# Optimization experiments

Hardware: AMD Instinct MI355X
Metric: run time of the kernel (lower is better)

The kernel has to match this reference:

```python
import jax, jax.numpy as jnp
import numpy as np

MAX_LENGTH = 13
PAD_TOKEN = 0
HIDDEN = 1024
VOCAB = 32000
BATCH = 64


def gru_cell(x, h, w_ih, w_hh, b_ih, b_hh):
    # PyTorch GRU gate order: reset, update, new
    gi = x @ w_ih.T + b_ih            # [B, 3H]
    gh = h @ w_hh.T + b_hh            # [B, 3H]
    i_r, i_z, i_n = jnp.split(gi, 3, axis=-1)
    h_r, h_z, h_n = jnp.split(gh, 3, axis=-1)
    r = jax.nn.sigmoid(i_r + h_r)
    z = jax.nn.sigmoid(i_z + h_z)
    n = jnp.tanh(i_n + r * h_n)
    return (1.0 - z) * n + z * h


def setup_inputs() -> dict:
    key = jax.random.key(0)
    ks = jax.random.split(key, 9)
    s = 0.02
    return {
        "encoder_outputs": jax.random.normal(ks[0], (BATCH, MAX_LENGTH, HIDDEN), jnp.float32),
        "encoder_hidden": jax.random.normal(ks[1], (1, BATCH, HIDDEN), jnp.float32),
        "embedding": jax.random.normal(ks[2], (VOCAB, HIDDEN), jnp.float32) * s,
        "w_ih": jax.random.normal(ks[3], (3 * HIDDEN, HIDDEN), jnp.float32) * s,
        "w_hh": jax.random.normal(ks[4], (3 * HIDDEN, HIDDEN), jnp.float32) * s,
        "b_ih": jnp.zeros((3 * HIDDEN,), jnp.float32),
        "b_hh": jnp.zeros((3 * HIDDEN,), jnp.float32),
        "w_out": jax.random.normal(ks[5], (VOCAB, HIDDEN), jnp.float32) * s,
        "b_out": jnp.zeros((VOCAB,), jnp.float32),
    }


def reference(encoder_outputs, encoder_hidden, embedding, w_ih, w_hh, b_ih, b_hh, w_out, b_out):
    batch = encoder_outputs.shape[0]
    h0 = encoder_hidden[0]                               # [B, H]
    tok0 = jnp.full((batch,), PAD_TOKEN, dtype=jnp.int32)

    def step(carry, _):
        h, tok = carry
        x = jax.nn.relu(embedding[tok])                  # embed + relu
        h = gru_cell(x, h, w_ih, w_hh, b_ih, b_hh)       # GRU cell
        logits = h @ w_out.T + b_out                     # [B, V]
        nxt = jnp.argmax(logits, axis=-1).astype(jnp.int32)  # greedy feedback (topk(1))
        return (h, nxt), logits

    (h_final, _), logits = jax.lax.scan(step, (h0, tok0), None, length=MAX_LENGTH)
    logits = jnp.transpose(logits, (1, 0, 2))            # [B, T, V]
    log_probs = jax.nn.log_softmax(logits, axis=-1)
    return log_probs, h_final[None]
```

## Files before the change

### kernel.cpp

```cpp
#include <hip/hip_runtime.h>
#include <math.h>

#define BB 64
#define HH 1024
#define VV 32000
#define TT 13
#define QS 8000
#define BKL 128

typedef float f32x4 __attribute__((ext_vector_type(4)));
typedef __bf16 bf16x8 __attribute__((ext_vector_type(8)));

__device__ __forceinline__ unsigned short f2bf(float f) {
  unsigned u = __float_as_uint(f);
  u = (u + 0x7fffu + ((u >> 16) & 1u)) >> 16;
  return (unsigned short)u;
}
__device__ __forceinline__ float bf2f(unsigned short s) {
  return __uint_as_float(((unsigned)s) << 16);
}

__device__ __forceinline__ void gld16(const void* g, void* l) {
  __builtin_amdgcn_global_load_lds(
      (const __attribute__((address_space(1))) unsigned int*)g,
      (__attribute__((address_space(3))) unsigned int*)l, 16, 0, 0);
}

__global__ __launch_bounds__(1024) void k_init(
    const float* __restrict__ enc, const float* __restrict__ emb,
    float* __restrict__ hrm, unsigned short* __restrict__ hhi,
    unsigned short* __restrict__ hlo, unsigned short* __restrict__ xhi,
    unsigned short* __restrict__ xlo) {
  const int g = blockIdx.x * 1024 + threadIdx.x;
  const float h = enc[g];
  hrm[g] = h;
  const unsigned short h16 = f2bf(h);
  hhi[g] = h16;
  hlo[g] = f2bf(h - bf2f(h16));
  float e = emb[threadIdx.x];
  e = e > 0.f ? e : 0.f;
  const unsigned short e16 = f2bf(e);
  xhi[g] = e16;
  xlo[g] = f2bf(e - bf2f(e16));
}

__global__ __launch_bounds__(256) void k_wconv(const float* __restrict__ w,
                                               unsigned short* __restrict__ o) {
  const int n4 = VV * HH / 4;
  for (int i = blockIdx.x * 256 + threadIdx.x; i < n4; i += gridDim.x * 256) {
    const f32x4 v = ((const f32x4*)w)[i];
    ushort4 u;
    u.x = f2bf(v[0]); u.y = f2bf(v[1]); u.z = f2bf(v[2]); u.w = f2bf(v[3]);
    ((ushort4*)o)[i] = u;
  }
}

__global__ __launch_bounds__(256) void k_wconv2(
    const float* __restrict__ wih, const float* __restrict__ whh,
    unsigned short* __restrict__ ghi, unsigned short* __restrict__ glo) {
  const int n4 = 6 * HH * HH / 4;
  for (int i = blockIdx.x * 256 + threadIdx.x; i < n4; i += gridDim.x * 256) {
    const int flat = i * 4;
    const float* src = flat < 3 * HH * HH ? wih + flat : whh + (flat - 3 * HH * HH);
    const f32x4 v = *(const f32x4*)src;
    ushort4 hi, lo;
    hi.x = f2bf(v[0]); lo.x = f2bf(v[0] - bf2f(hi.x));
    hi.y = f2bf(v[1]); lo.y = f2bf(v[1] - bf2f(hi.y));
    hi.z = f2bf(v[2]); lo.z = f2bf(v[2] - bf2f(hi.z));
    hi.w = f2bf(v[3]); lo.w = f2bf(v[3] - bf2f(hi.w));
    ((ushort4*)ghi)[i] = hi;
    ((ushort4*)glo)[i] = lo;
  }
}

__global__ __launch_bounds__(256) void k_wconv3(
    const float* __restrict__ emb, unsigned short* __restrict__ ehi,
    unsigned short* __restrict__ elo) {
  const int n4 = VV * HH / 4;
  for (int i = blockIdx.x * 256 + threadIdx.x; i < n4; i += gridDim.x * 256) {
    f32x4 v = ((const f32x4*)emb)[i];
    #pragma unroll
    for (int u = 0; u < 4; ++u) v[u] = v[u] > 0.f ? v[u] : 0.f;
    ushort4 hi, lo;
    hi.x = f2bf(v[0]); lo.x = f2bf(v[0] - bf2f(hi.x));
    hi.y = f2bf(v[1]); lo.y = f2bf(v[1] - bf2f(hi.y));
    hi.z = f2bf(v[2]); lo.z = f2bf(v[2] - bf2f(hi.z));
    hi.w = f2bf(v[3]); lo.w = f2bf(v[3] - bf2f(hi.w));
    ((ushort4*)ehi)[i] = hi;
    ((ushort4*)elo)[i] = lo;
  }
}

__global__ __launch_bounds__(64) void k_gruG(
    const unsigned short* __restrict__ ehi, const unsigned short* __restrict__ elo,
    const unsigned short* __restrict__ hhi_s, const unsigned short* __restrict__ hlo_s,
    const unsigned short* __restrict__ ghi, const unsigned short* __restrict__ glo,
    const float* __restrict__ qbestV, const int* __restrict__ qbestI,
    float* __restrict__ gbuf, int use_qbest) {
  __shared__ int stok[64];
  const int blk = blockIdx.x, lane = threadIdx.x;
  const int kh = blk & 1;
  const int r2 = blk >> 1;
  const int g6 = r2 % 6, jt = r2 / 6;
  const int cl = lane & 15, kk = (lane >> 4) * 8;
  const int j = jt * 16 + cl;
  const int kbeg = kh * 512;
  const bool ih = g6 < 3;

  if (ih) {
    int tok = 0;
    if (use_qbest) {
      float bv = qbestV[lane * 4 + 0]; int bi = qbestI[lane * 4 + 0];
      #pragma unroll
      for (int qq = 1; qq < 4; ++qq) {
        const float v = qbestV[lane * 4 + qq]; const int i2 = qbestI[lane * 4 + qq];
        if (v > bv || (v == bv && i2 < bi)) { bv = v; bi = i2; }
      }
      tok = bi;
    }
    stok[lane] = tok;
  }
  __syncthreads();

  size_t abase[4];
  #pragma unroll
  for (int rt = 0; rt < 4; ++rt) {
    const int row = rt * 16 + cl;
    abase[rt] = (ih ? (size_t)stok[row] : (size_t)row) * HH + kbeg + kk;
  }
  const unsigned short* Ahi = ih ? ehi : hhi_s;
  const unsigned short* Alo = ih ? elo : hlo_s;
  const unsigned short* bh = ghi + (size_t)(g6 * HH + j) * HH + kbeg;
  const unsigned short* bl = glo + (size_t)(g6 * HH + j) * HH + kbeg;

  f32x4 acc[4];
  acc[0] = acc[1] = acc[2] = acc[3] = (f32x4){0.f, 0.f, 0.f, 0.f};
  #pragma unroll 4
  for (int k0 = 0; k0 < 512; k0 += 32) {
    const bf16x8 whi = *(const bf16x8*)(bh + k0 + kk);
    const bf16x8 wlo = *(const bf16x8*)(bl + k0 + kk);
    #pragma unroll
    for (int rt = 0; rt < 4; ++rt) {
      const bf16x8 a_h = *(const bf16x8*)(Ahi + abase[rt] + k0);
      const bf16x8 a_l = *(const bf16x8*)(Alo + abase[rt] + k0);
      acc[rt] = __builtin_amdgcn_mfma_f32_16x16x32_bf16(a_h, whi, acc[rt], 0, 0, 0);
      acc[rt] = __builtin_amdgcn_mfma_f32_16x16x32_bf16(a_l, whi, acc[rt], 0, 0, 0);
      acc[rt] = __builtin_amdgcn_mfma_f32_16x16x32_bf16(a_h, wlo, acc[rt], 0, 0, 0);
    }
  }
  #pragma unroll
  for (int rt = 0; rt < 4; ++rt)
    #pragma unroll
    for (int rg = 0; rg < 4; ++rg) {
      const int row = rt * 16 + (lane >> 4) * 4 + rg;
      gbuf[(size_t)((kh * 6 + g6) * BB + row) * HH + jt * 16 + cl] = acc[rt][rg];
    }
}

__global__ __launch_bounds__(256) void k_gepO(
    const float* __restrict__ gbuf, const float* __restrict__ bih,
    const float* __restrict__ bhh, const float* __restrict__ hsrc,
    float* __restrict__ hdst, unsigned short* __restrict__ hhi_d,
    unsigned short* __restrict__ hlo_d,
    const float* __restrict__ lbufPrev, const float* __restrict__ mq,
    const float* __restrict__ sq, float* __restrict__ out, int t) {
  __shared__ float lz[BB];
  const int tid = threadIdx.x;
  const int gid = blockIdx.x * 256 + tid;
  if (t > 0 && tid < BB) {
    const int b = tid;
    const float m0 = mq[b * 4 + 0], m1 = mq[b * 4 + 1];
    const float m2 = mq[b * 4 + 2], m3 = mq[b * 4 + 3];
    const float Mg = fmaxf(fmaxf(m0, m1), fmaxf(m2, m3));
    const float Sg = sq[b * 4 + 0] * __expf(m0 - Mg) + sq[b * 4 + 1] * __expf(m1 - Mg) +
                     sq[b * 4 + 2] * __expf(m2 - Mg) + sq[b * 4 + 3] * __expf(m3 - Mg);
    lz[b] = Mg + logf(Sg);
  }
  __syncthreads();
  {
    const int b = gid >> 10, j = gid & (HH - 1);
    const size_t base = (size_t)b * HH + j;
    const float gir = gbuf[(size_t)(0 * BB + b) * HH + j] + gbuf[(size_t)((6 + 0) * BB + b) * HH + j] + bih[j];
    const float giz = gbuf[(size_t)(1 * BB + b) * HH + j] + gbuf[(size_t)((6 + 1) * BB + b) * HH + j] + bih[HH + j];
    const float gin = gbuf[(size_t)(2 * BB + b) * HH + j] + gbuf[(size_t)((6 + 2) * BB + b) * HH + j] + bih[2 * HH + j];
    const float ghr = gbuf[(size_t)(3 * BB + b) * HH + j] + gbuf[(size_t)((6 + 3) * BB + b) * HH + j] + bhh[j];
    const float ghz = gbuf[(size_t)(4 * BB + b) * HH + j] + gbuf[(size_t)((6 + 4) * BB + b) * HH + j] + bhh[HH + j];
    const float ghn = gbuf[(size_t)(5 * BB + b) * HH + j] + gbuf[(size_t)((6 + 5) * BB + b) * HH + j] + bhh[2 * HH + j];
    const float r_ = 1.f / (1.f + __expf(-(gir + ghr)));
    const float z_ = 1.f / (1.f + __expf(-(giz + ghz)));
    const float n_ = tanhf(gin + r_ * ghn);
    const float hnew = (1.f - z_) * n_ + z_ * hsrc[base];
    hdst[base] = hnew;
    const unsigned short h16 = f2bf(hnew);
    hhi_d[base] = h16;
    hlo_d[base] = f2bf(hnew - bf2f(h16));
  }
  if (t > 0) {
    const f32x4* src = (const f32x4*)lbufPrev;
    for (int i4 = gid; i4 < BB * VV / 4; i4 += 65536) {
      const int b = i4 / (VV / 4);
      const f32x4 v = src[i4];
      ((f32x4*)out)[(size_t)(b * TT + (t - 1)) * (VV / 4) + (i4 - b * (VV / 4))] = v - lz[b];
    }
  }
}

__global__ __launch_bounds__(512, 1) void k_logits_lds(
    const unsigned short* __restrict__ hb,
    const unsigned short* __restrict__ wbf,
    const float* __restrict__ bout, float* __restrict__ lbuf) {
  __shared__ __attribute__((aligned(16))) unsigned char sA[2][64 * BKL * 2];
  __shared__ __attribute__((aligned(16))) unsigned char sB[2][128 * BKL * 2];
  const int tid = threadIdx.x, blk = blockIdx.x;
  const int lane = tid & 63, wv = tid >> 6;
  const int cl = lane & 15, kk = (lane >> 4) * 8;

  auto STAGE = [&](int buf, int k0) {
    #pragma unroll
    for (int it = 0; it < 2; ++it) {
      const int c = it * 512 + tid;
      const int r = c >> 4;
      const int kb = (c & 15) * 16;
      const int kbs = kb ^ ((r & 7) << 4);
      gld16(hb + (size_t)r * HH + k0 + (kbs >> 1),
            &sA[buf][it * 8192 + wv * 1024]);
    }
    #pragma unroll
    for (int it = 0; it < 4; ++it) {
      const int c = it * 512 + tid;
      const int col = c >> 4;
      const int kb = (c & 15) * 16;
      const int kbs = kb ^ ((col & 7) << 4);
      gld16(wbf + (size_t)(blk * 128 + col) * HH + k0 + (kbs >> 1),
            &sB[buf][it * 8192 + wv * 1024]);
    }
  };

  f32x4 acc[4];
  acc[0] = acc[1] = acc[2] = acc[3] = (f32x4){0.f, 0.f, 0.f, 0.f};

  STAGE(0, 0);
  for (int t = 0; t < HH / BKL; ++t) {
    const int cur = t & 1;
    if (t < HH / BKL - 1) {
      STAGE(cur ^ 1, (t + 1) * BKL);
      asm volatile("s_waitcnt vmcnt(6)" ::: "memory");
    } else {
      asm volatile("s_waitcnt vmcnt(0)" ::: "memory");
    }
    __builtin_amdgcn_s_barrier();
    __builtin_amdgcn_sched_barrier(0);
    #pragma unroll
    for (int ks = 0; ks < BKL; ks += 32) {
      const int bc = wv * 16 + cl;
      const bf16x8 bfr = *(const bf16x8*)&sB[cur][bc * (BKL * 2) + (((ks + kk) * 2) ^ ((bc & 7) << 4))];
      #pragma unroll
      for (int rt = 0; rt < 4; ++rt) {
        const int ar = rt * 16 + cl;
        const bf16x8 afr = *(const bf16x8*)&sA[cur][ar * (BKL * 2) + (((ks + kk) * 2) ^ ((ar & 7) << 4))];
        acc[rt] = __builtin_amdgcn_mfma_f32_16x16x32_bf16(afr, bfr, acc[rt], 0, 0, 0);
      }
    }
    __builtin_amdgcn_s_barrier();
    __builtin_amdgcn_sched_barrier(0);
  }

  const int col = blk * 128 + wv * 16 + cl;
  const float bo = bout[col];
  #pragma unroll
  for (int rt = 0; rt < 4; ++rt)
    #pragma unroll
    for (int rg = 0; rg < 4; ++rg) {
      const int row = rt * 16 + (lane >> 4) * 4 + rg;
      lbuf[(size_t)row * VV + col] = acc[rt][rg] + bo;
    }
}

__global__ __launch_bounds__(256) void k_sum(
    const float* __restrict__ lbuf, const float* __restrict__ wout,
    const float* __restrict__ bout, const float* __restrict__ hnew,
    float* __restrict__ mq, float* __restrict__ sq,
    float* __restrict__ qbestV, int* __restrict__ qbestI, int dorecheck) {
  __shared__ float srow[QS];
  __shared__ float red[4];
  __shared__ int icnt;
  __shared__ int scand[32];
  const int tid = threadIdx.x;
  const int b = blockIdx.x >> 2, q = blockIdx.x & 3;
  const int lane = tid & 63, wv = tid >> 6;
  const f32x4* src = (const f32x4*)(lbuf + (size_t)b * VV + q * QS);
  f32x4* s4 = (f32x4*)srow;

  float m = -3.0e38f;
  for (int i = tid; i < QS / 4; i += 256) {
    const f32x4 v = src[i];
    s4[i] = v;
    m = fmaxf(fmaxf(fmaxf(m, v[0]), v[1]), fmaxf(v[2], v[3]));
  }
  #pragma unroll
  for (int d = 1; d < 64; d <<= 1) m = fmaxf(m, __shfl_xor(m, d, 64));
  if (lane == 0) red[wv] = m;
  if (tid == 0) icnt = 0;
  __syncthreads();
  const float M = fmaxf(fmaxf(red[0], red[1]), fmaxf(red[2], red[3]));

  float s = 0.f;
  for (int i = tid; i < QS / 4; i += 256) {
    const f32x4 v = s4[i];
    s += __expf(v[0] - M) + __expf(v[1] - M) + __expf(v[2] - M) + __expf(v[3] - M);
  }
  #pragma unroll
  for (int d = 1; d < 64; d <<= 1) s += __shfl_xor(s, d, 64);
  __syncthreads();
  if (lane == 0) red[wv] = s;
  __syncthreads();
  if (tid == 0) {
    mq[b * 4 + q] = M;
    sq[b * 4 + q] = red[0] + red[1] + red[2] + red[3];
  }

  if (dorecheck) {
    const float thr = M - 0.05f;
    for (int i = tid; i < QS / 4; i += 256) {
      const f32x4 v = s4[i];
      #pragma unroll
      for (int u = 0; u < 4; ++u)
        if (v[u] >= thr) {
          const int c = atomicAdd(&icnt, 1);
          if (c < 32) scand[c] = q * QS + 4 * i + u;
        }
    }
    __syncthreads();
    if (wv == 0) {
      const int nc = icnt < 32 ? icnt : 32;
      const float* hrow = hnew + (size_t)b * HH;
      f32x4 h4[4];
      #pragma unroll
      for (int u = 0; u < 4; ++u) h4[u] = *(const f32x4*)(hrow + lane * 16 + u * 4);
      float best = -3.0e38f; int bi = 0x7fffffff;
      for (int ci = 0; ci < nc; ++ci) {
        const int v = scand[ci];
        const float* wrow = wout + (size_t)v * HH + lane * 16;
        float ss = 0.f;
        #pragma unroll
        for (int u = 0; u < 4; ++u) {
          const f32x4 w4 = *(const f32x4*)(wrow + u * 4);
          ss += h4[u][0] * w4[0] + h4[u][1] * w4[1] + h4[u][2] * w4[2] + h4[u][3] * w4[3];
        }
        #pragma unroll
        for (int d = 1; d < 64; d <<= 1) ss += __shfl_xor(ss, d, 64);
        ss += bout[v];
        if (ss > best || (ss == best && v < bi)) { best = ss; bi = v; }
      }
      if (lane == 0) { qbestV[b * 4 + q] = best; qbestI[b * 4 + q] = bi; }
    }
  }
}

__global__ __launch_bounds__(256) void k_fin(
    const float* __restrict__ lbufLast, const float* __restrict__ mq,
    const float* __restrict__ sq, const float* __restrict__ hfin,
    float* __restrict__ out) {
  __shared__ float lz[BB];
  const int tid = threadIdx.x;
  const int gid = blockIdx.x * 256 + tid;
  if (tid < BB) {
    const int b = tid;
    const float m0 = mq[b * 4 + 0], m1 = mq[b * 4 + 1];
    const float m2 = mq[b * 4 + 2], m3 = mq[b * 4 + 3];
    const float Mg = fmaxf(fmaxf(m0, m1), fmaxf(m2, m3));
    const float Sg = sq[b * 4 + 0] * __expf(m0 - Mg) + sq[b * 4 + 1] * __expf(m1 - Mg) +
                     sq[b * 4 + 2] * __expf(m2 - Mg) + sq[b * 4 + 3] * __expf(m3 - Mg);
    lz[b] = Mg + logf(Sg);
  }
  __syncthreads();
  const f32x4* src = (const f32x4*)lbufLast;
  for (int i4 = gid; i4 < BB * VV / 4; i4 += 65536) {
    const int b = i4 / (VV / 4);
    const f32x4 v = src[i4];
    ((f32x4*)out)[(size_t)(b * TT + (TT - 1)) * (VV / 4) + (i4 - b * (VV / 4))] = v - lz[b];
  }
  out[(size_t)BB * TT * VV + gid] = hfin[gid];
}

__global__ __launch_bounds__(64) void k_gru_fb(
    const unsigned short* __restrict__ xhi, const unsigned short* __restrict__ xlo,
    const unsigned short* __restrict__ hhi_s, const unsigned short* __restrict__ hlo_s,
    const float* __restrict__ wih, const float* __restrict__ whh,
    float* __restrict__ gbuf) {
  const int blk = blockIdx.x, lane = threadIdx.x;
  const int kh = blk & 1;
  const int r2 = blk >> 1;
  const int g6 = r2 % 6, jt = r2 / 6;
  const unsigned short* Ahi = g6 < 3 ? xhi : hhi_s;
  const unsigned short* Alo = g6 < 3 ? xlo : hlo_s;
  const int cl = lane & 15, kk = (lane >> 4) * 8;
  const int j = jt * 16 + cl;
  const int kbeg = kh * 512;
  f32x4 acc[4];
  acc[0] = acc[1] = acc[2] = acc[3] = (f32x4){0.f, 0.f, 0.f, 0.f};
  const float* W = (g6 < 3 ? wih : whh) + (size_t)((g6 % 3) * HH + j) * HH + kbeg;
  for (int k0 = 0; k0 < 512; k0 += 32) {
    const f32x4 w0 = *(const f32x4*)(W + k0 + kk);
    const f32x4 w1 = *(const f32x4*)(W + k0 + kk + 4);
    union { unsigned short u[8]; bf16x8 b; } chi, clo;
    #pragma unroll
    for (int u2 = 0; u2 < 4; ++u2) {
      chi.u[u2] = f2bf(w0[u2]); clo.u[u2] = f2bf(w0[u2] - bf2f(chi.u[u2]));
      chi.u[4 + u2] = f2bf(w1[u2]); clo.u[4 + u2] = f2bf(w1[u2] - bf2f(chi.u[4 + u2]));
    }
    #pragma unroll
    for (int rt = 0; rt < 4; ++rt) {
      const size_t aoff = (size_t)(rt * 16 + cl) * HH + kbeg + k0 + kk;
      const bf16x8 a_h = *(const bf16x8*)(Ahi + aoff);
      const bf16x8 a_l = *(const bf16x8*)(Alo + aoff);
      acc[rt] = __builtin_amdgcn_mfma_f32_16x16x32_bf16(a_h, chi.b, acc[rt], 0, 0, 0);
      acc[rt] = __builtin_amdgcn_mfma_f32_16x16x32_bf16(a_l, chi.b, acc[rt], 0, 0, 0);
      acc[rt] = __builtin_amdgcn_mfma_f32_16x16x32_bf16(a_h, clo.b, acc[rt], 0, 0, 0);
    }
  }
  #pragma unroll
  for (int rt = 0; rt < 4; ++rt)
    #pragma unroll
    for (int rg = 0; rg < 4; ++rg) {
      const int row = rt * 16 + (lane >> 4) * 4 + rg;
      gbuf[(size_t)((kh * 6 + g6) * BB + row) * HH + jt * 16 + cl] = acc[rt][rg];
    }
}

__global__ __launch_bounds__(256) void k_gep_fb(
    const float* __restrict__ gbuf, const float* __restrict__ bih,
    const float* __restrict__ bhh, const float* __restrict__ hsrc,
    float* __restrict__ hdst, unsigned short* __restrict__ hhi_d,
    unsigned short* __restrict__ hlo_d) {
  const int e = blockIdx.x * 256 + threadIdx.x;
  const int b = e >> 10, j = e & (HH - 1);
  const size_t base = (size_t)b * HH + j;
  const float gir = gbuf[(size_t)(0 * BB + b) * HH + j] + gbuf[(size_t)((6 + 0) * BB + b) * HH + j] + bih[j];
  const float giz = gbuf[(size_t)(1 * BB + b) * HH + j] + gbuf[(size_t)((6 + 1) * BB + b) * HH + j] + bih[HH + j];
  const float gin = gbuf[(size_t)(2 * BB + b) * HH + j] + gbuf[(size_t)((6 + 2) * BB + b) * HH + j] + bih[2 * HH + j];
  const float ghr = gbuf[(size_t)(3 * BB + b) * HH + j] + gbuf[(size_t)((6 + 3) * BB + b) * HH + j] + bhh[j];
  const float ghz = gbuf[(size_t)(4 * BB + b) * HH + j] + gbuf[(size_t)((6 + 4) * BB + b) * HH + j] + bhh[HH + j];
  const float ghn = gbuf[(size_t)(5 * BB + b) * HH + j] + gbuf[(size_t)((6 + 5) * BB + b) * HH + j] + bhh[2 * HH + j];
  const float r_ = 1.f / (1.f + __expf(-(gir + ghr)));
  const float z_ = 1.f / (1.f + __expf(-(giz + ghz)));
  const float n_ = tanhf(gin + r_ * ghn);
  const float hnew = (1.f - z_) * n_ + z_ * hsrc[base];
  hdst[base] = hnew;
  const unsigned short h16 = f2bf(hnew);
  hhi_d[base] = h16;
  hlo_d[base] = f2bf(hnew - bf2f(h16));
}

__global__ __launch_bounds__(256) void k_logits_fb(
    const unsigned short* __restrict__ hb, const float* __restrict__ wout,
    const float* __restrict__ bout, float* __restrict__ lbuf) {
  const int tid = threadIdx.x, blk = blockIdx.x;
  const int lane = tid & 63, wv = tid >> 6;
  const int n0 = blk * 64 + wv * 16;
  const int cl = lane & 15, kk = (lane >> 4) * 8;
  f32x4 acc[4];
  acc[0] = acc[1] = acc[2] = acc[3] = (f32x4){0.f, 0.f, 0.f, 0.f};
  const float* wrow = wout + (size_t)(n0 + cl) * HH;
  for (int k0 = 0; k0 < HH; k0 += 32) {
    const f32x4 w0 = *(const f32x4*)(wrow + k0 + kk);
    const f32x4 w1 = *(const f32x4*)(wrow + k0 + kk + 4);
    union { unsigned short u[8]; bf16x8 b; } cv;
    #pragma unroll
    for (int u2 = 0; u2 < 4; ++u2) { cv.u[u2] = f2bf(w0[u2]); cv.u[4 + u2] = f2bf(w1[u2]); }
    #pragma unroll
    for (int rt = 0; rt < 4; ++rt) {
      const bf16x8 afr = *(const bf16x8*)(hb + (size_t)(rt * 16 + cl) * HH + k0 + kk);
      acc[rt] = __builtin_amdgcn_mfma_f32_16x16x32_bf16(afr, cv.b, acc[rt], 0, 0, 0);
    }
  }
  const int col = n0 + cl;
  const float bo = bout[col];
  #pragma unroll
  for (int rt = 0; rt < 4; ++rt)
    #pragma unroll
    for (int rg = 0; rg < 4; ++rg) {
      const int row = rt * 16 + (lane >> 4) * 4 + rg;
      lbuf[(size_t)row * VV + col] = acc[rt][rg] + bo;
    }
}

__global__ __launch_bounds__(256) void k_out_fb(
    const float* __restrict__ lbuf, const float* __restrict__ mq,
    const float* __restrict__ sq, const float* __restrict__ qbestV,
    const int* __restrict__ qbestI, const float* __restrict__ emb,
    const float* __restrict__ hnew, float* __restrict__ out,
    unsigned short* __restrict__ xhi, unsigned short* __restrict__ xlo, int t) {
  __shared__ int stok;
  const int tid = threadIdx.x;
  const int b = blockIdx.x >> 2, q = blockIdx.x & 3;
  const float m0 = mq[b * 4 + 0], m1 = mq[b * 4 + 1];
  const float m2 = mq[b * 4 + 2], m3 = mq[b * 4 + 3];
  const float Mg = fmaxf(fmaxf(m0, m1), fmaxf(m2, m3));
  const float Sg = sq[b * 4 + 0] * __expf(m0 - Mg) + sq[b * 4 + 1] * __expf(m1 - Mg) +
                   sq[b * 4 + 2] * __expf(m2 - Mg) + sq[b * 4 + 3] * __expf(m3 - Mg);
  const float LZ = Mg + logf(Sg);
  const f32x4* src = (const f32x4*)(lbuf + (size_t)b * VV + q * QS);
  f32x4* dst = (f32x4*)(out + ((size_t)b * TT + t) * VV + q * QS);
  for (int i = tid; i < QS / 4; i += 256)
    dst[i] = src[i] - LZ;
  if (q == 0 && t < TT - 1) {
    if (tid == 0) {
      float bv = qbestV[b * 4 + 0]; int bi = qbestI[b * 4 + 0];
      #pragma unroll
      for (int qq = 1; qq < 4; ++qq) {
        const float v = qbestV[b * 4 + qq]; const int i2 = qbestI[b * 4 + qq];
        if (v > bv || (v == bv && i2 < bi)) { bv = v; bi = i2; }
      }
      stok = bi;
    }
    __syncthreads();
    const int tok = stok;
    for (int j = tid; j < HH; j += 256) {
      float e = emb[(size_t)tok * HH + j];
      e = e > 0.f ? e : 0.f;
      const unsigned short e16 = f2bf(e);
      xhi[(size_t)b * HH + j] = e16;
      xlo[(size_t)b * HH + j] = f2bf(e - bf2f(e16));
    }
  }
  if (q == 0 && t == TT - 1) {
    for (int j = tid; j < HH; j += 256)
      out[(size_t)BB * TT * VV + (size_t)b * HH + j] = hnew[(size_t)b * HH + j];
  }
}

extern "C" void kernel_launch(void* const* d_in, const int* in_sizes, int n_in,
                              void* d_out, int out_size, void* d_ws, size_t ws_size,
                              hipStream_t stream) {
  const float* enc  = (const float*)d_in[1];
  const float* emb  = (const float*)d_in[2];
  const float* wih  = (const float*)d_in[3];
  const float* whh  = (const float*)d_in[4];
  const float* bih  = (const float*)d_in[5];
  const float* bhh  = (const float*)d_in[6];
  const float* wout = (const float*)d_in[7];
  const float* bout = (const float*)d_in[8];
  float* out = (float*)d_out;

  char* ws = (char*)d_ws;
  size_t off = 0;
  auto alloc = [&](size_t bytes) -> char* {
    char* p = ws + off;
    off += (bytes + 255) & ~(size_t)255;
    return p;
  };
  float* hrm = (float*)alloc((size_t)2 * BB * HH * 4);
  unsigned short* hhi = (unsigned short*)alloc((size_t)2 * BB * HH * 2);
  unsigned short* hlo = (unsigned short*)alloc((size_t)2 * BB * HH * 2);
  unsigned short* xhi = (unsigned short*)alloc((size_t)BB * HH * 2);
  unsigned short* xlo = (unsigned short*)alloc((size_t)BB * HH * 2);
  float* gbuf = (float*)alloc((size_t)12 * BB * HH * 4);
  float* lbuf = (float*)alloc((size_t)2 * BB * VV * 4);
  float* mq = (float*)alloc((size_t)BB * 4 * 4);
  float* sq = (float*)alloc((size_t)BB * 4 * 4);
  float* qbestV = (float*)alloc((size_t)BB * 4 * 4);
  int* qbestI = (int*)alloc((size_t)BB * 4 * 4);
  unsigned short* wbf = (unsigned short*)alloc((size_t)VV * HH * 2);
  unsigned short* ghi = (unsigned short*)alloc((size_t)6 * HH * HH * 2);
  unsigned short* glo = (unsigned short*)alloc((size_t)6 * HH * HH * 2);
  unsigned short* ehi = (unsigned short*)alloc((size_t)VV * HH * 2);
  unsigned short* elo = (unsigned short*)alloc((size_t)VV * HH * 2);
  const int cache_ok = (ws_size >= off) ? 1 : 0;

  hipLaunchKernelGGL(k_init, dim3(64), dim3(1024), 0, stream,
                     enc, emb, hrm, hhi, hlo, xhi, xlo);
  if (cache_ok) {
    hipLaunchKernelGGL(k_wconv, dim3(2048), dim3(256), 0, stream, wout, wbf);
    hipLaunchKernelGGL(k_wconv2, dim3(1024), dim3(256), 0, stream, wih, whh, ghi, glo);
    hipLaunchKernelGGL(k_wconv3, dim3(2048), dim3(256), 0, stream, emb, ehi, elo);
  }

  for (int t = 0; t < TT; ++t) {
    const int p = t & 1;
    const float* hsrc = hrm + (size_t)p * BB * HH;
    float* hdst = hrm + (size_t)(p ^ 1) * BB * HH;
    const unsigned short* hhs = hhi + (size_t)p * BB * HH;
    const unsigned short* hls = hlo + (size_t)p * BB * HH;
    unsigned short* hhd = hhi + (size_t)(p ^ 1) * BB * HH;
    unsigned short* hld = hlo + (size_t)(p ^ 1) * BB * HH;
    float* lb = lbuf + (size_t)(t & 1) * BB * VV;
    const float* lbPrev = lbuf + (size_t)((t & 1) ^ 1) * BB * VV;

    if (cache_ok) {
      hipLaunchKernelGGL(k_gruG, dim3(768), dim3(64), 0, stream,
                         ehi, elo, hhs, hls, ghi, glo, qbestV, qbestI,
                         gbuf, (t > 0) ? 1 : 0);
      hipLaunchKernelGGL(k_gepO, dim3(256), dim3(256), 0, stream,
                         gbuf, bih, bhh, hsrc, hdst, hhd, hld,
                         lbPrev, mq, sq, out, t);
      hipLaunchKernelGGL(k_logits_lds, dim3(250), dim3(512), 0, stream,
                         hhd, wbf, bout, lb);
      hipLaunchKernelGGL(k_sum, dim3(256), dim3(256), 0, stream,
                         lb, wout, bout, hdst, mq, sq, qbestV, qbestI,
                         (t < TT - 1) ? 1 : 0);
    } else {
      hipLaunchKernelGGL(k_gru_fb, dim3(768), dim3(64), 0, stream,
                         xhi, xlo, hhs, hls, wih, whh, gbuf);
      hipLaunchKernelGGL(k_gep_fb, dim3(256), dim3(256), 0, stream,
                         gbuf, bih, bhh, hsrc, hdst, hhd, hld);
      hipLaunchKernelGGL(k_logits_fb, dim3(500), dim3(256), 0, stream,
                         hhd, wout, bout, lb);
      hipLaunchKernelGGL(k_sum, dim3(256), dim3(256), 0, stream,
                         lb, wout, bout, hdst, mq, sq, qbestV, qbestI,
                         (t < TT - 1) ? 1 : 0);
      hipLaunchKernelGGL(k_out_fb, dim3(256), dim3(256), 0, stream,
                         lb, mq, sq, qbestV, qbestI, emb, hdst, out, xhi, xlo, t);
    }
  }

  if (cache_ok)
    hipLaunchKernelGGL(k_fin, dim3(256), dim3(256), 0, stream,
                       lbuf + (size_t)((TT - 1) & 1) * BB * VV, mq, sq,
                       hrm + (size_t)BB * HH, out);
}
```

Baseline: 1.115 ms.

## Drop full embedding bf16 split; convert only per-quarter candidate rows in k_sum

Removes the k_wconv3 pass, which converted the entire 32000x1024 embedding table into hi/lo bf16 arrays on every call. Instead, each k_sum block converts the ReLU'd embedding row of its quarter-best token into a small per-(batch,quarter) staging buffer. k_gru then picks the winning quarter's row through a quarter index rather than a token index. This saves a large memory pass and about 256MB of workspace writes, at the cost of extra row conversions and a barrier inside k_sum on every step.

```diff
diff --git a/kernel.cpp b/kernel.cpp
--- a/kernel.cpp
+++ b/kernel.cpp
@@ -29,19 +29,24 @@
 __global__ __launch_bounds__(1024) void k_init(
     const float* __restrict__ enc, const float* __restrict__ emb,
     float* __restrict__ hrm, unsigned short* __restrict__ hhi,
-    unsigned short* __restrict__ hlo, unsigned short* __restrict__ xhi,
-    unsigned short* __restrict__ xlo) {
-  const int g = blockIdx.x * 1024 + threadIdx.x;
+    unsigned short* __restrict__ hlo,
+    unsigned short* __restrict__ xhi_c, unsigned short* __restrict__ xlo_c,
+    unsigned short* __restrict__ xhi0, unsigned short* __restrict__ xlo0) {
+  const int b = blockIdx.x, tid = threadIdx.x;
+  const int g = b * 1024 + tid;
   const float h = enc[g];
   hrm[g] = h;
   const unsigned short h16 = f2bf(h);
   hhi[g] = h16;
   hlo[g] = f2bf(h - bf2f(h16));
-  float e = emb[threadIdx.x];
+  float e = emb[tid];
   e = e > 0.f ? e : 0.f;
   const unsigned short e16 = f2bf(e);
-  xhi[g] = e16;
-  xlo[g] = f2bf(e - bf2f(e16));
+  const unsigned short el16 = f2bf(e - bf2f(e16));
+  xhi_c[(size_t)(b * 4 + 0) * HH + tid] = e16;
+  xlo_c[(size_t)(b * 4 + 0) * HH + tid] = el16;
+  xhi0[g] = e16;
+  xlo0[g] = el16;
 }
 
 __global__ __launch_bounds__(256) void k_wconv(const float* __restrict__ w,
@@ -73,31 +78,13 @@
   }
 }
 
-__global__ __launch_bounds__(256) void k_wconv3(
-    const float* __restrict__ emb, unsigned short* __restrict__ ehi,
-    unsigned short* __restrict__ elo) {
-  const int n4 = VV * HH / 4;
-  for (int i = blockIdx.x * 256 + threadIdx.x; i < n4; i += gridDim.x * 256) {
-    f32x4 v = ((const f32x4*)emb)[i];
-    #pragma unroll
-    for (int u = 0; u < 4; ++u) v[u] = v[u] > 0.f ? v[u] : 0.f;
-    ushort4 hi, lo;
-    hi.x = f2bf(v[0]); lo.x = f2bf(v[0] - bf2f(hi.x));
-    hi.y = f2bf(v[1]); lo.y = f2bf(v[1] - bf2f(hi.y));
-    hi.z = f2bf(v[2]); lo.z = f2bf(v[2] - bf2f(hi.z));
-    hi.w = f2bf(v[3]); lo.w = f2bf(v[3] - bf2f(hi.w));
-    ((ushort4*)ehi)[i] = hi;
-    ((ushort4*)elo)[i] = lo;
-  }
-}
-
-__global__ __launch_bounds__(64) void k_gruG(
-    const unsigned short* __restrict__ ehi, const unsigned short* __restrict__ elo,
+__global__ __launch_bounds__(64) void k_gru(
+    const unsigned short* __restrict__ xhi_c, const unsigned short* __restrict__ xlo_c,
     const unsigned short* __restrict__ hhi_s, const unsigned short* __restrict__ hlo_s,
     const unsigned short* __restrict__ ghi, const unsigned short* __restrict__ glo,
     const float* __restrict__ qbestV, const int* __restrict__ qbestI,
     float* __restrict__ gbuf, int use_qbest) {
-  __shared__ int stok[64];
+  __shared__ int squart[64];
   const int blk = blockIdx.x, lane = threadIdx.x;
   const int kh = blk & 1;
   const int r2 = blk >> 1;
@@ -108,17 +95,16 @@
   const bool ih = g6 < 3;
 
   if (ih) {
-    int tok = 0;
+    int qw = 0;
     if (use_qbest) {
       float bv = qbestV[lane * 4 + 0]; int bi = qbestI[lane * 4 + 0];
       #pragma unroll
       for (int qq = 1; qq < 4; ++qq) {
         const float v = qbestV[lane * 4 + qq]; const int i2 = qbestI[lane * 4 + qq];
-        if (v > bv || (v == bv && i2 < bi)) { bv = v; bi = i2; }
+        if (v > bv || (v == bv && i2 < bi)) { bv = v; bi = i2; qw = qq; }
       }
-      tok = bi;
-    }
-    stok[lane] = tok;
+    }
+    squart[lane] = qw;
   }
   __syncthreads();
 
@@ -126,10 +112,10 @@
   #pragma unroll
   for (int rt = 0; rt < 4; ++rt) {
     const int row = rt * 16 + cl;
-    abase[rt] = (ih ? (size_t)stok[row] : (size_t)row) * HH + kbeg + kk;
-  }
-  const unsigned short* Ahi = ih ? ehi : hhi_s;
-  const unsigned short* Alo = ih ? elo : hlo_s;
+    abase[rt] = (ih ? (size_t)(row * 4 + squart[row]) : (size_t)row) * HH + kbeg + kk;
+  }
+  const unsigned short* Ahi = ih ? xhi_c : hhi_s;
+  const unsigned short* Alo = ih ? xlo_c : hlo_s;
   const unsigned short* bh = ghi + (size_t)(g6 * HH + j) * HH + kbeg;
   const unsigned short* bl = glo + (size_t)(g6 * HH + j) * HH + kbeg;
 
@@ -279,11 +265,14 @@
 __global__ __launch_bounds__(256) void k_sum(
     const float* __restrict__ lbuf, const float* __restrict__ wout,
     const float* __restrict__ bout, const float* __restrict__ hnew,
+    const float* __restrict__ emb,
     float* __restrict__ mq, float* __restrict__ sq,
-    float* __restrict__ qbestV, int* __restrict__ qbestI, int dorecheck) {
+    float* __restrict__ qbestV, int* __restrict__ qbestI,
+    unsigned short* __restrict__ xhi_c, unsigned short* __restrict__ xlo_c,
+    int dorecheck) {
   __shared__ float srow[QS];
   __shared__ float red[4];
-  __shared__ int icnt;
+  __shared__ int icnt, sbi;
   __shared__ int scand[32];
   const int tid = threadIdx.x;
   const int b = blockIdx.x >> 2, q = blockIdx.x & 3;
@@ -352,7 +341,24 @@
         ss += bout[v];
         if (ss > best || (ss == best && v < bi)) { best = ss; bi = v; }
       }
-      if (lane == 0) { qbestV[b * 4 + q] = best; qbestI[b * 4 + q] = bi; }
+      if (lane == 0) { qbestV[b * 4 + q] = best; qbestI[b * 4 + q] = bi; sbi = bi; }
+    }
+    __syncthreads();
+    const int bi = sbi;
+    const float* erow = emb + (size_t)bi * HH;
+    unsigned short* xh = xhi_c + (size_t)(b * 4 + q) * HH;
+    unsigned short* xl = xlo_c + (size_t)(b * 4 + q) * HH;
+    for (int k = tid; k < HH / 4; k += 256) {
+      f32x4 v = ((const f32x4*)erow)[k];
+      ushort4 hi, lo;
+      #pragma unroll
+      for (int u = 0; u < 4; ++u) v[u] = v[u] > 0.f ? v[u] : 0.f;
+      hi.x = f2bf(v[0]); lo.x = f2bf(v[0] - bf2f(hi.x));
+      hi.y = f2bf(v[1]); lo.y = f2bf(v[1] - bf2f(hi.y));
+      hi.z = f2bf(v[2]); lo.z = f2bf(v[2] - bf2f(hi.z));
+      hi.w = f2bf(v[3]); lo.w = f2bf(v[3] - bf2f(hi.w));
+      ((ushort4*)xh)[k] = hi;
+      ((ushort4*)xl)[k] = lo;
     }
   }
 }
@@ -553,8 +559,10 @@
   float* hrm = (float*)alloc((size_t)2 * BB * HH * 4);
   unsigned short* hhi = (unsigned short*)alloc((size_t)2 * BB * HH * 2);
   unsigned short* hlo = (unsigned short*)alloc((size_t)2 * BB * HH * 2);
-  unsigned short* xhi = (unsigned short*)alloc((size_t)BB * HH * 2);
-  unsigned short* xlo = (unsigned short*)alloc((size_t)BB * HH * 2);
+  unsigned short* xhi_c = (unsigned short*)alloc((size_t)BB * 4 * HH * 2);
+  unsigned short* xlo_c = (unsigned short*)alloc((size_t)BB * 4 * HH * 2);
+  unsigned short* xhi0 = (unsigned short*)alloc((size_t)BB * HH * 2);
+  unsigned short* xlo0 = (unsigned short*)alloc((size_t)BB * HH * 2);
   float* gbuf = (float*)alloc((size_t)12 * BB * HH * 4);
   float* lbuf = (float*)alloc((size_t)2 * BB * VV * 4);
   float* mq = (float*)alloc((size_t)BB * 4 * 4);
@@ -564,32 +572,27 @@
   unsigned short* wbf = (unsigned short*)alloc((size_t)VV * HH * 2);
   unsigned short* ghi = (unsigned short*)alloc((size_t)6 * HH * HH * 2);
   unsigned short* glo = (unsigned short*)alloc((size_t)6 * HH * HH * 2);
-  unsigned short* ehi = (unsigned short*)alloc((size_t)VV * HH * 2);
-  unsigned short* elo = (unsigned short*)alloc((size_t)VV * HH * 2);
   const int cache_ok = (ws_size >= off) ? 1 : 0;
 
   hipLaunchKernelGGL(k_init, dim3(64), dim3(1024), 0, stream,
-                     enc, emb, hrm, hhi, hlo, xhi, xlo);
+                     enc, emb, hrm, hhi, hlo, xhi_c, xlo_c, xhi0, xlo0);
   if (cache_ok) {
     hipLaunchKernelGGL(k_wconv, dim3(2048), dim3(256), 0, stream, wout, wbf);
     hipLaunchKernelGGL(k_wconv2, dim3(1024), dim3(256), 0, stream, wih, whh, ghi, glo);
-    hipLaunchKernelGGL(k_wconv3, dim3(2048), dim3(256), 0, stream, emb, ehi, elo);
-  }
-
-  for (int t = 0; t < TT; ++t) {
-    const int p = t & 1;
-    const float* hsrc = hrm + (size_t)p * BB * HH;
-    float* hdst = hrm + (size_t)(p ^ 1) * BB * HH;
-    const unsigned short* hhs = hhi + (size_t)p * BB * HH;
-    const unsigned short* hls = hlo + (size_t)p * BB * HH;
-    unsigned short* hhd = hhi + (size_t)(p ^ 1) * BB * HH;
-    unsigned short* hld = hlo + (size_t)(p ^ 1) * BB * HH;
-    float* lb = lbuf + (size_t)(t & 1) * BB * VV;
-    const float* lbPrev = lbuf + (size_t)((t & 1) ^ 1) * BB * VV;
-
-    if (cache_ok) {
-      hipLaunchKernelGGL(k_gruG, dim3(768), dim3(64), 0, stream,
-                         ehi, elo, hhs, hls, ghi, glo, qbestV, qbestI,
+
+    for (int t = 0; t < TT; ++t) {
+      const int p = t & 1;
+      const float* hsrc = hrm + (size_t)p * BB * HH;
+      float* hdst = hrm + (size_t)(p ^ 1) * BB * HH;
+      const unsigned short* hhs = hhi + (size_t)p * BB * HH;
+      const unsigned short* hls = hlo + (size_t)p * BB * HH;
+      unsigned short* hhd = hhi + (size_t)(p ^ 1) * BB * HH;
+      unsigned short* hld = hlo + (size_t)(p ^ 1) * BB * HH;
+      float* lb = lbuf + (size_t)(t & 1) * BB * VV;
+      const float* lbPrev = lbuf + (size_t)((t & 1) ^ 1) * BB * VV;
+
+      hipLaunchKernelGGL(k_gru, dim3(768), dim3(64), 0, stream,
+                         xhi_c, xlo_c, hhs, hls, ghi, glo, qbestV, qbestI,
                          gbuf, (t > 0) ? 1 : 0);
       hipLaunchKernelGGL(k_gepO, dim3(256), dim3(256), 0, stream,
                          gbuf, bih, bhh, hsrc, hdst, hhd, hld,
@@ -597,25 +600,33 @@
       hipLaunchKernelGGL(k_logits_lds, dim3(250), dim3(512), 0, stream,
                          hhd, wbf, bout, lb);
       hipLaunchKernelGGL(k_sum, dim3(256), dim3(256), 0, stream,
-                         lb, wout, bout, hdst, mq, sq, qbestV, qbestI,
-                         (t < TT - 1) ? 1 : 0);
-    } else {
+                         lb, wout, bout, hdst, emb, mq, sq, qbestV, qbestI,
+                         xhi_c, xlo_c, (t < TT - 1) ? 1 : 0);
+    }
+    hipLaunchKernelGGL(k_fin, dim3(256), dim3(256), 0, stream,
+                       lbuf + (size_t)((TT - 1) & 1) * BB * VV, mq, sq,
+                       hrm + (size_t)BB * HH, out);
+  } else {
+    float* lb0 = lbuf;
+    for (int t = 0; t < TT; ++t) {
+      const int p = t & 1;
+      const float* hsrc = hrm + (size_t)p * BB * HH;
+      float* hdst = hrm + (size_t)(p ^ 1) * BB * HH;
+      const unsigned short* hhs = hhi + (size_t)p * BB * HH;
+      const unsigned short* hls = hlo + (size_t)p * BB * HH;
+      unsigned short* hhd = hhi + (size_t)(p ^ 1) * BB * HH;
+      unsigned short* hld = hlo + (size_t)(p ^ 1) * BB * HH;
       hipLaunchKernelGGL(k_gru_fb, dim3(768), dim3(64), 0, stream,
-                         xhi, xlo, hhs, hls, wih, whh, gbuf);
+                         xhi0, xlo0, hhs, hls, wih, whh, gbuf);
       hipLaunchKernelGGL(k_gep_fb, dim3(256), dim3(256), 0, stream,
                          gbuf, bih, bhh, hsrc, hdst, hhd, hld);
       hipLaunchKernelGGL(k_logits_fb, dim3(500), dim3(256), 0, stream,
-                         hhd, wout, bout, lb);
+                         hhd, wout, bout, lb0);
       hipLaunchKernelGGL(k_sum, dim3(256), dim3(256), 0, stream,
-                         lb, wout, bout, hdst, mq, sq, qbestV, qbestI,
-                         (t < TT - 1) ? 1 : 0);
+                         lb0, wout, bout, hdst, emb, mq, sq, qbestV, qbestI,
+                         xhi_c, xlo_c, (t < TT - 1) ? 1 : 0);
       hipLaunchKernelGGL(k_out_fb, dim3(256), dim3(256), 0, stream,
-                         lb, mq, sq, qbestV, qbestI, emb, hdst, out, xhi, xlo, t);
-    }
-  }
-
-  if (cache_ok)
-    hipLaunchKernelGGL(k_fin, dim3(256), dim3(256), 0, stream,
-                       lbuf + (size_t)((TT - 1) & 1) * BB * VV, mq, sq,
-                       hrm + (size_t)BB * HH, out);
-}
+                         lb0, mq, sq, qbestV, qbestI, emb, hdst, out, xhi0, xlo0, t);
+    }
+  }
+}
```

Measured after the change: 966.2 us. 13.3% less time.
